# Kernel tuning notes

Measured on AMD Instinct MI355X. Metric: run time of the kernel, lower is better.

## Reference

```python
import jax, jax.numpy as jnp
import numpy as np

KSIZE = 3  # median window

def median_blur(x, k):
    # x: [B, C, H, W]; zero padding (k-1)//2, median over k*k window
    # (matches kornia's conv2d-with-binary-kernels + median implementation)
    p = (k - 1) // 2
    xp = jnp.pad(x, ((0, 0), (0, 0), (p, p), (p, p)))
    B, C, H, W = x.shape
    # stack k*k shifted views -> [B, C, H, W, k*k] (k*k=9, small static loop)
    patches = jnp.stack(
        [xp[:, :, i:i + H, j:j + W] for i in range(k) for j in range(k)],
        axis=-1,
    )
    return jnp.median(patches, axis=-1)


def setup_inputs() -> dict:
    key = jax.random.key(0)
    k1, k2, k3 = jax.random.split(key, 3)
    B, C, H, W = 32, 256, 64, 64
    x = jax.random.normal(k1, (B, C, H, W), dtype=jnp.float32)
    # 1x1 conv weight [out_c, in_c] (the trailing 1x1 spatial dims are squeezed)
    conv_w = jax.random.normal(k2, (C, C), dtype=jnp.float32) * (1.0 / np.sqrt(C))
    conv_b = jax.random.normal(k3, (C,), dtype=jnp.float32) * 0.01
    return {"x": x, "conv_w": conv_w, "conv_b": conv_b}


def reference(x, conv_w, conv_b):
    x_denoised = median_blur(x, KSIZE)  # [B, C, H, W]
    # 1x1 conv == per-pixel channel mixing GEMM
    conv_out = jnp.einsum("oc,bchw->bohw", conv_w, x_denoised) + conv_b[None, :, None, None]
    return x + conv_out
```

## Files before the change

kernel.cpp:

```cpp
#include <hip/hip_runtime.h>

typedef float f32x4 __attribute__((ext_vector_type(4)));
typedef __bf16 bf16x8 __attribute__((ext_vector_type(8)));
typedef unsigned short u16x8 __attribute__((ext_vector_type(8)));

__device__ __forceinline__ unsigned short f2bf(float f) {
  union { float f; unsigned u; } v; v.f = f;
  unsigned r = v.u + 0x7FFFu + ((v.u >> 16) & 1u);
  return (unsigned short)(r >> 16);
}

__device__ __forceinline__ float min3f(float a, float b, float c) {
  return fminf(fminf(a, b), c);
}
__device__ __forceinline__ float max3f(float a, float b, float c) {
  return fmaxf(fmaxf(a, b), c);
}
__device__ __forceinline__ float med3f(float a, float b, float c) {
  return __builtin_amdgcn_fmed3f(a, b, c);
}

__global__ void wconv_k(const float* __restrict__ w, unsigned short* __restrict__ wbf) {
  int idx  = blockIdx.x * 256 + threadIdx.x;
  int lane = idx & 63;
  int ob   = (idx >> 6) & 15;
  int ks   = idx >> 10;
  int o = (ob << 4) + (lane & 15);
  int c = (ks << 5) + ((lane >> 4) << 3);
  const float* src = w + (o << 8) + c;
  f32x4 v0 = *(const f32x4*)src;
  f32x4 v1 = *(const f32x4*)(src + 4);
  u16x8 ov;
  ov[0] = f2bf(v0[0]); ov[1] = f2bf(v0[1]); ov[2] = f2bf(v0[2]); ov[3] = f2bf(v0[3]);
  ov[4] = f2bf(v1[0]); ov[5] = f2bf(v1[1]); ov[6] = f2bf(v1[2]); ov[7] = f2bf(v1[3]);
  *(u16x8*)(wbf + (idx << 3)) = ov;
}

__launch_bounds__(256, 2)
__global__ void fused_k(const float* __restrict__ x,
                        const unsigned short* __restrict__ wbf,
                        const float* __restrict__ bias,
                        float* __restrict__ out) {
  __shared__ unsigned short Bt[2][64][40];
  __shared__ float BiasS[256];

  const int t   = threadIdx.x;
  const int blk = blockIdx.x;
  const int swz = ((blk & 7) << 8) | (blk >> 3);
  const int b   = swz >> 6;
  const int r   = swz & 63;
  const int lane = t & 63;
  const int w    = t >> 6;
  const int g    = lane >> 4;
  const int l15  = lane & 15;

  const int ci  = t >> 3;
  const int s   = t & 7;
  const int px0 = s << 3;
  const int cw  = ci ^ ((s & 3) << 3);

  BiasS[t] = bias[t];

  const float* xb = x + ((size_t)b << 20);
  const bool rT = (r >= 1), rB = (r <= 62);
  const bool hasL = (s > 0), hasR = (s < 7);
  const float* pbase = xb + ((size_t)ci << 12) + (r << 6) + px0;

  f32x4 acc[4][4];
  #pragma unroll
  for (int m = 0; m < 4; ++m)
    #pragma unroll
    for (int n = 0; n < 4; ++n)
      acc[m][n] = (f32x4){0.f, 0.f, 0.f, 0.f};

  f32x4 pf[3][6];

  auto load_strip = [&](int step, f32x4* dst) {
    const float* p = pbase + ((size_t)(step << 5) << 12);
    dst[0] = dst[1] = dst[4] = dst[5] = (f32x4){0.f, 0.f, 0.f, 0.f};
    if (rT) { dst[0] = *(const f32x4*)(p - 64); dst[1] = *(const f32x4*)(p - 60); }
    dst[2] = *(const f32x4*)p;       dst[3] = *(const f32x4*)(p + 4);
    if (rB) { dst[4] = *(const f32x4*)(p + 64); dst[5] = *(const f32x4*)(p + 68); }
  };

  auto median_store = [&](const f32x4* C, int buf) {
    float tl = __shfl_up(C[1][3], 1);
    float ml = __shfl_up(C[3][3], 1);
    float bl = __shfl_up(C[5][3], 1);
    float tr = __shfl_down(C[0][0], 1);
    float mr = __shfl_down(C[2][0], 1);
    float br = __shfl_down(C[4][0], 1);
    float R0[10], R1[10], R2[10];
    R0[0] = hasL ? tl : 0.f;  R1[0] = hasL ? ml : 0.f;  R2[0] = hasL ? bl : 0.f;
    R0[9] = hasR ? tr : 0.f;  R1[9] = hasR ? mr : 0.f;  R2[9] = hasR ? br : 0.f;
    #pragma unroll
    for (int j = 0; j < 4; ++j) {
      R0[1 + j] = C[0][j];  R0[5 + j] = C[1][j];
      R1[1 + j] = C[2][j];  R1[5 + j] = C[3][j];
      R2[1 + j] = C[4][j];  R2[5 + j] = C[5][j];
    }
    float mn[10], md[10], mx[10];
    #pragma unroll
    for (int j = 0; j < 10; ++j) {
      mn[j] = min3f(R0[j], R1[j], R2[j]);
      md[j] = med3f(R0[j], R1[j], R2[j]);
      mx[j] = max3f(R0[j], R1[j], R2[j]);
    }
    #pragma unroll
    for (int i = 0; i < 8; ++i) {
      float t0 = max3f(mn[i], mn[i+1], mn[i+2]);
      float t1 = med3f(md[i], md[i+1], md[i+2]);
      float t2 = min3f(mx[i], mx[i+1], mx[i+2]);
      Bt[buf][px0 + i][cw] = f2bf(med3f(t0, t1, t2));
    }
  };

  load_strip(0, pf[0]);
  load_strip(1, pf[1]);
  load_strip(2, pf[2]);
  median_store(pf[0], 0);
  __syncthreads();

  #pragma unroll
  for (int ks = 0; ks < 8; ++ks) {
    bf16x8 bb[4];
    #pragma unroll
    for (int n = 0; n < 4; ++n) {
      const int px = (n << 4) + l15;
      const int gc = (g ^ ((px >> 3) & 3)) << 3;
      bb[n] = __builtin_bit_cast(bf16x8, *(const u16x8*)&Bt[ks & 1][px][gc]);
    }
    bf16x8 a[4];
    #pragma unroll
    for (int m = 0; m < 4; ++m) {
      const int fidx = (((ks << 4) + (w << 2) + m) << 6) + lane;
      a[m] = __builtin_bit_cast(bf16x8, *(const u16x8*)(wbf + ((size_t)fidx << 3)));
    }
    if (ks <= 4) load_strip(ks + 3, pf[ks % 3]);
    if (ks < 7) median_store(pf[(ks + 1) % 3], (ks + 1) & 1);

    #pragma unroll
    for (int m = 0; m < 4; ++m)
      #pragma unroll
      for (int n = 0; n < 4; ++n)
        acc[m][n] = __builtin_amdgcn_mfma_f32_16x16x32_bf16(a[m], bb[n], acc[m][n], 0, 0, 0);

    if (ks < 7) __syncthreads();
  }

  #pragma unroll
  for (int m = 0; m < 4; ++m) {
    const int o = (w << 6) + (m << 4) + (g << 2);
    #pragma unroll
    for (int n = 0; n < 4; ++n) {
      const int px = (n << 4) + l15;
      const size_t base = ((((size_t)b << 8) + (size_t)o) << 12) + ((size_t)r << 6) + (size_t)px;
      #pragma unroll
      for (int q = 0; q < 4; ++q) {
        const size_t idx = base + ((size_t)q << 12);
        out[idx] = x[idx] + acc[m][n][q] + BiasS[o + q];
      }
    }
  }
}

extern "C" void kernel_launch(void* const* d_in, const int* in_sizes, int n_in,
                              void* d_out, int out_size, void* d_ws, size_t ws_size,
                              hipStream_t stream) {
  const float* x  = (const float*)d_in[0];
  const float* cw = (const float*)d_in[1];
  const float* cb = (const float*)d_in[2];
  float* out = (float*)d_out;
  unsigned short* wbf = (unsigned short*)d_ws;

  hipLaunchKernelGGL(wconv_k, dim3(32), dim3(256), 0, stream, cw, wbf);
  hipLaunchKernelGGL(fused_k, dim3(2048), dim3(256), 0, stream, x, wbf, cb, out);
}
```

Baseline: 76.74 us.

## Stage input strips into LDS via direct global-to-LDS loads, raise occupancy

The median stage no longer loads each 3-row strip into registers with a three-deep prefetch. Each k-step's 32-channel by 3-row input tile is now copied straight into an XOR-swizzled LDS buffer with global_load_lds, and the next tile's loads are issued right after the barrier so they overlap the MFMA phase. The bf16 median tile becomes a single buffer, and launch bounds go from 2 to 3 blocks per CU to use the freed registers. The price is more LDS traffic, an extra barrier per step, and reliance on correct wait counts for the asynchronous LDS writes.

```diff
diff --git a/kernel.cpp b/kernel.cpp
--- a/kernel.cpp
+++ b/kernel.cpp
@@ -18,6 +18,12 @@
 }
 __device__ __forceinline__ float med3f(float a, float b, float c) {
   return __builtin_amdgcn_fmed3f(a, b, c);
+}
+
+__device__ __forceinline__ void gload_lds16(const void* g, void* l) {
+  __builtin_amdgcn_global_load_lds(
+      (const __attribute__((address_space(1))) void*)g,
+      (__attribute__((address_space(3))) void*)l, 16, 0, 0);
 }
 
 __global__ void wconv_k(const float* __restrict__ w, unsigned short* __restrict__ wbf) {
@@ -36,12 +42,13 @@
   *(u16x8*)(wbf + (idx << 3)) = ov;
 }
 
-__launch_bounds__(256, 2)
+__launch_bounds__(256, 3)
 __global__ void fused_k(const float* __restrict__ x,
                         const unsigned short* __restrict__ wbf,
                         const float* __restrict__ bias,
                         float* __restrict__ out) {
-  __shared__ unsigned short Bt[2][64][40];
+  __shared__ float Xs[96][64];
+  __shared__ unsigned short Bt[64][40];
   __shared__ float BiasS[256];
 
   const int t   = threadIdx.x;
@@ -58,13 +65,28 @@
   const int s   = t & 7;
   const int px0 = s << 3;
   const int cw  = ci ^ ((s & 3) << 3);
-
-  BiasS[t] = bias[t];
-
-  const float* xb = x + ((size_t)b << 20);
   const bool rT = (r >= 1), rB = (r <= 62);
   const bool hasL = (s > 0), hasR = (s < 7);
-  const float* pbase = xb + ((size_t)ci << 12) + (r << 6) + px0;
+
+  BiasS[t] = bias[t];
+
+  const float* xb = x + ((size_t)b << 20);
+
+  unsigned soff[6];
+  #pragma unroll
+  for (int p = 0; p < 6; ++p) {
+    int row = w * 24 + (p << 2) + (lane >> 4);
+    int cip = (row * 171) >> 9;
+    int drp = row - cip * 3;
+    int gr  = r + drp - 1;
+    gr = gr < 0 ? 0 : (gr > 63 ? 63 : gr);
+    int bG  = (lane & 15) ^ (cip & 7);
+    soff[p] = ((unsigned)cip << 14) + ((unsigned)gr << 8) + ((unsigned)bG << 4);
+  }
+
+  #pragma unroll
+  for (int p = 0; p < 6; ++p)
+    gload_lds16((const char*)xb + soff[p], &Xs[w * 24 + (p << 2)][0]);
 
   f32x4 acc[4][4];
   #pragma unroll
@@ -73,72 +95,75 @@
     for (int n = 0; n < 4; ++n)
       acc[m][n] = (f32x4){0.f, 0.f, 0.f, 0.f};
 
-  f32x4 pf[3][6];
-
-  auto load_strip = [&](int step, f32x4* dst) {
-    const float* p = pbase + ((size_t)(step << 5) << 12);
-    dst[0] = dst[1] = dst[4] = dst[5] = (f32x4){0.f, 0.f, 0.f, 0.f};
-    if (rT) { dst[0] = *(const f32x4*)(p - 64); dst[1] = *(const f32x4*)(p - 60); }
-    dst[2] = *(const f32x4*)p;       dst[3] = *(const f32x4*)(p + 4);
-    if (rB) { dst[4] = *(const f32x4*)(p + 64); dst[5] = *(const f32x4*)(p + 68); }
-  };
-
-  auto median_store = [&](const f32x4* C, int buf) {
-    float tl = __shfl_up(C[1][3], 1);
-    float ml = __shfl_up(C[3][3], 1);
-    float bl = __shfl_up(C[5][3], 1);
-    float tr = __shfl_down(C[0][0], 1);
-    float mr = __shfl_down(C[2][0], 1);
-    float br = __shfl_down(C[4][0], 1);
-    float R0[10], R1[10], R2[10];
-    R0[0] = hasL ? tl : 0.f;  R1[0] = hasL ? ml : 0.f;  R2[0] = hasL ? bl : 0.f;
-    R0[9] = hasR ? tr : 0.f;  R1[9] = hasR ? mr : 0.f;  R2[9] = hasR ? br : 0.f;
-    #pragma unroll
-    for (int j = 0; j < 4; ++j) {
-      R0[1 + j] = C[0][j];  R0[5 + j] = C[1][j];
-      R1[1 + j] = C[2][j];  R1[5 + j] = C[3][j];
-      R2[1 + j] = C[4][j];  R2[5 + j] = C[5][j];
-    }
+  const int ri0 = ci * 3;
+  const int sig = ci & 7;
+  const int bAi = ((s << 1)) ^ sig;
+  const int bBi = ((s << 1) | 1) ^ sig;
+  const int bLi = (((s << 1) - 1) & 15) ^ sig;
+  const int bRi = (((s << 1) + 2) & 15) ^ sig;
+
+  __syncthreads();
+
+  #pragma unroll
+  for (int ks = 0; ks < 8; ++ks) {
+    bf16x8 a[4];
+    #pragma unroll
+    for (int m = 0; m < 4; ++m) {
+      const int fidx = (((ks << 4) + (w << 2) + m) << 6) + lane;
+      a[m] = __builtin_bit_cast(bf16x8, *(const u16x8*)(wbf + ((size_t)fidx << 3)));
+    }
+
+    float R[3][10];
+    #pragma unroll
+    for (int dr = 0; dr < 3; ++dr) {
+      const float* rp = &Xs[ri0 + dr][0];
+      f32x4 va = *(const f32x4*)(rp + (bAi << 2));
+      f32x4 vb = *(const f32x4*)(rp + (bBi << 2));
+      R[dr][0] = hasL ? rp[(bLi << 2) + 3] : 0.f;
+      R[dr][9] = hasR ? rp[(bRi << 2)]     : 0.f;
+      #pragma unroll
+      for (int j = 0; j < 4; ++j) { R[dr][1 + j] = va[j]; R[dr][5 + j] = vb[j]; }
+    }
+    if (!rT) {
+      #pragma unroll
+      for (int j = 0; j < 10; ++j) R[0][j] = 0.f;
+    }
+    if (!rB) {
+      #pragma unroll
+      for (int j = 0; j < 10; ++j) R[2][j] = 0.f;
+    }
+
     float mn[10], md[10], mx[10];
     #pragma unroll
     for (int j = 0; j < 10; ++j) {
-      mn[j] = min3f(R0[j], R1[j], R2[j]);
-      md[j] = med3f(R0[j], R1[j], R2[j]);
-      mx[j] = max3f(R0[j], R1[j], R2[j]);
+      mn[j] = min3f(R[0][j], R[1][j], R[2][j]);
+      md[j] = med3f(R[0][j], R[1][j], R[2][j]);
+      mx[j] = max3f(R[0][j], R[1][j], R[2][j]);
     }
     #pragma unroll
     for (int i = 0; i < 8; ++i) {
       float t0 = max3f(mn[i], mn[i+1], mn[i+2]);
       float t1 = med3f(md[i], md[i+1], md[i+2]);
       float t2 = min3f(mx[i], mx[i+1], mx[i+2]);
-      Bt[buf][px0 + i][cw] = f2bf(med3f(t0, t1, t2));
-    }
-  };
-
-  load_strip(0, pf[0]);
-  load_strip(1, pf[1]);
-  load_strip(2, pf[2]);
-  median_store(pf[0], 0);
-  __syncthreads();
-
-  #pragma unroll
-  for (int ks = 0; ks < 8; ++ks) {
+      Bt[px0 + i][cw] = f2bf(med3f(t0, t1, t2));
+    }
+
+    __syncthreads();
+
+    if (ks < 7) {
+      const unsigned kso = (unsigned)(ks + 1) << 19;
+      #pragma unroll
+      for (int p = 0; p < 6; ++p)
+        gload_lds16((const char*)xb + (soff[p] + kso), &Xs[w * 24 + (p << 2)][0]);
+    }
+
     bf16x8 bb[4];
     #pragma unroll
     for (int n = 0; n < 4; ++n) {
       const int px = (n << 4) + l15;
       const int gc = (g ^ ((px >> 3) & 3)) << 3;
-      bb[n] = __builtin_bit_cast(bf16x8, *(const u16x8*)&Bt[ks & 1][px][gc]);
-    }
-    bf16x8 a[4];
-    #pragma unroll
-    for (int m = 0; m < 4; ++m) {
-      const int fidx = (((ks << 4) + (w << 2) + m) << 6) + lane;
-      a[m] = __builtin_bit_cast(bf16x8, *(const u16x8*)(wbf + ((size_t)fidx << 3)));
-    }
-    if (ks <= 4) load_strip(ks + 3, pf[ks % 3]);
-    if (ks < 7) median_store(pf[(ks + 1) % 3], (ks + 1) & 1);
-
+      bb[n] = __builtin_bit_cast(bf16x8, *(const u16x8*)&Bt[px][gc]);
+    }
     #pragma unroll
     for (int m = 0; m < 4; ++m)
       #pragma unroll
```

Measured after the change: 74.09 us. -3.5%, faster.
